# Kernel optimization log

Measured on AMD Instinct MI355X. Metric: run time of the kernel, lower is better.

Reference implementation:

```python
import jax, jax.numpy as jnp
import numpy as np

NUM_SINGERS = 1024
EMB = 63
H = 256
FEAT = 1 + EMB  # 64


def setup_inputs() -> dict:
    key = jax.random.key(0)
    ks = jax.random.split(key, 16)
    B, T = 32, 2048
    s = 0.05
    return {
        "duration_input": jax.random.uniform(ks[0], (B, T), jnp.float32),
        "sid_input": jax.random.randint(ks[1], (B, T), 0, NUM_SINGERS),
        "embed": jax.random.normal(ks[2], (NUM_SINGERS, EMB), jnp.float32) * s,
        "Wi_f": jax.random.normal(ks[3], (FEAT, 3 * H), jnp.float32) * s,
        "Wh_f": jax.random.normal(ks[4], (H, 3 * H), jnp.float32) * s,
        "bi_f": jnp.zeros((3 * H,), jnp.float32),
        "bhn_f": jnp.zeros((H,), jnp.float32),
        "Wi_b": jax.random.normal(ks[5], (FEAT, 3 * H), jnp.float32) * s,
        "Wh_b": jax.random.normal(ks[6], (H, 3 * H), jnp.float32) * s,
        "bi_b": jnp.zeros((3 * H,), jnp.float32),
        "bhn_b": jnp.zeros((H,), jnp.float32),
        "Wd": jax.random.normal(ks[7], (2 * H, 1), jnp.float32) * s,
        "bd": jnp.zeros((1,), jnp.float32),
    }


def _gru(x_tbf, Wi, Wh, bi, bhn):
    # x_tbf: [T, B, F]; flax GRUCell math: r/z recurrent dense without bias,
    # n = tanh(in + r*(Wh_n h + bhn)); h' = (1-z)*n + z*h
    gi = jnp.einsum("tbf,fh->tbh", x_tbf, Wi) + bi  # precompute input gates [T,B,3H]

    def step(h, gi_t):
        gh = h @ Wh  # [B, 3H]
        ir, iz, inn = jnp.split(gi_t, 3, axis=-1)
        hr, hz, hn = jnp.split(gh, 3, axis=-1)
        r = jax.nn.sigmoid(ir + hr)
        z = jax.nn.sigmoid(iz + hz)
        n = jnp.tanh(inn + r * (hn + bhn))
        h_new = (1.0 - z) * n + z * h
        return h_new, h_new

    B = x_tbf.shape[1]
    h0 = jnp.zeros((B, H), x_tbf.dtype)
    _, ys = jax.lax.scan(step, h0, gi)
    return ys  # [T, B, H]


def reference(duration_input, sid_input, embed, Wi_f, Wh_f, bi_f, bhn_f,
              Wi_b, Wh_b, bi_b, bhn_b, Wd, bd):
    sid_emb = embed[sid_input]  # [B, T, EMB]
    feats = jnp.concatenate([duration_input[..., None], sid_emb], axis=-1)  # [B,T,F]
    x = jnp.transpose(feats, (1, 0, 2))  # [T, B, F]
    fwd = _gru(x, Wi_f, Wh_f, bi_f, bhn_f)                 # [T,B,H]
    bwd = _gru(x[::-1], Wi_b, Wh_b, bi_b, bhn_b)[::-1]      # [T,B,H]
    out = jnp.concatenate([fwd, bwd], axis=-1)              # [T,B,2H]
    out = jnp.transpose(out, (1, 0, 2))                     # [B,T,2H]
    return out @ Wd + bd                                    # [B,T,1]
```

## Files before the change

kernel.cpp:

```cpp
#include <hip/hip_runtime.h>
#include <hip/hip_bf16.h>

#define T_LEN 2048
#define BATCH 32
#define HDIM 256
#define H3 768
#define EMBD 63
#define NSING 1024

typedef _Float16 half2_t __attribute__((ext_vector_type(2)));

__device__ __forceinline__ float fdot2u(unsigned int a, unsigned int b, float c) {
  return __builtin_amdgcn_fdot2(__builtin_bit_cast(half2_t, a),
                                __builtin_bit_cast(half2_t, b), c, false);
}

#define DPP_ADD(x, ctrl)                                                      \
  (x) += __builtin_bit_cast(                                                  \
      float, __builtin_amdgcn_update_dpp(                                     \
                 0, __builtin_bit_cast(int, (x)), (ctrl), 0xf, 0xf, true))

__global__ __launch_bounds__(768) void precompute_P(
    const float* __restrict__ embed, const float* __restrict__ Wi,
    const float* __restrict__ bi, _Float16* __restrict__ P2) {
  const int s = blockIdx.x;
  const int jg = threadIdx.x;
  const int g = jg >> 8, jj = jg & 255;
  float acc = bi[jg];
  const float* er = embed + s * EMBD;
#pragma unroll
  for (int e = 0; e < EMBD; e++) acc += er[e] * Wi[(e + 1) * H3 + jg];
  P2[((size_t)g * NSING + s) * HDIM + jj] = (_Float16)acc;
}

__global__ __launch_bounds__(256) void pack_Wh(
    const float* __restrict__ Wh_f, const float* __restrict__ Wh_b,
    unsigned int* __restrict__ Whp) {
  const int bid = blockIdx.x;
  const int j = threadIdx.x;
  const int g = bid % 3;
  const int k2 = (bid / 3) & 63;
  const int half = (bid / 192) & 1;
  const int d = bid / 384;
  const float* Wh = d ? Wh_b : Wh_f;
  const int r0 = half * 128 + 2 * k2;
  half2_t hp;
  hp.x = (_Float16)Wh[r0 * H3 + g * 256 + j];
  hp.y = (_Float16)Wh[(r0 + 1) * H3 + g * 256 + j];
  Whp[(size_t)bid * 256 + j] = __builtin_bit_cast(unsigned int, hp);
}

__global__ __attribute__((amdgpu_flat_work_group_size(512, 512),
                          amdgpu_waves_per_eu(2, 2))) void gru_scan(
    const float* __restrict__ dur, const int* __restrict__ sid,
    const unsigned int* __restrict__ Whp,
    const float* __restrict__ Wi_f, const float* __restrict__ Wi_b,
    const float* __restrict__ bhn_f, const float* __restrict__ bhn_b,
    const float* __restrict__ Wd,
    const _Float16* __restrict__ P2,
    float* __restrict__ pred) {
  const int b = blockIdx.x & 31;
  const int dir = blockIdx.x >> 5;
  const int tid = threadIdx.x;
  const int j = tid & 255;
  const int half = tid >> 8;

  const float* __restrict__ Wi = dir ? Wi_b : Wi_f;
  const float* __restrict__ bhn = dir ? bhn_b : bhn_f;
  const _Float16* __restrict__ Pd = P2 + (size_t)dir * 3 * NSING * HDIM;

  __shared__ __align__(16) unsigned int h2buf[2][128];
  __shared__ float pbuf[3][256];
  
  unsigned int w[192];
  {
    const unsigned int* wp = Whp + ((size_t)(dir * 2 + half)) * 192 * 256 + j;
#pragma unroll
    for (int i = 0; i < 192; i++) w[i] = wp[i * 256];
  }
#pragma unroll
  for (int i = 0; i < 192; i++) asm volatile("" : "+v"(w[i]));

  const float wi0r = Wi[j], wi0z = Wi[HDIM + j], wi0n = Wi[2 * HDIM + j];
  const float wd = Wd[dir * HDIM + j];
  const float bhnj = bhn[j];

  if (tid < 128) h2buf[0][tid] = 0u;
  float h_prev = 0.f;

  const float* durb = dur + b * T_LEN;
  const int* sidb = sid + b * T_LEN;
  float* predb = pred + ((size_t)(dir * BATCH + b)) * T_LEN * 4;

  float p_r = 0.f, p_z = 0.f, p_n = 0.f;
  if (!half) {
    const int s0 = sidb[dir ? (T_LEN - 1) : 0];
    p_r = (float)Pd[(0 * NSING + s0) * HDIM + j];
    p_z = (float)Pd[(1 * NSING + s0) * HDIM + j];
    p_n = (float)Pd[(2 * NSING + s0) * HDIM + j];
  }
  __syncthreads();

#pragma unroll 1
  for (int t = 0; t < T_LEN; t++) {
    const int cur = t & 1;
    const int tt = dir ? (T_LEN - 1 - t) : t;
    const int tn = (t + 1 < T_LEN) ? (t + 1) : (T_LEN - 1);
    float q_r, q_z, q_n;
    if (!half) {
      const int s1 = sidb[dir ? (T_LEN - 1 - tn) : tn];
      q_r = (float)Pd[(0 * NSING + s1) * HDIM + j];
      q_z = (float)Pd[(1 * NSING + s1) * HDIM + j];
      q_n = (float)Pd[(2 * NSING + s1) * HDIM + j];
    }
    const float d_c = durb[tt];

    const uint4* hv4 = (const uint4*)&h2buf[cur][half * 64];
    float ar = 0, az = 0, an = 0, ar2 = 0, az2 = 0, an2 = 0;
#pragma unroll
    for (int kk = 0; kk < 16; kk++) {
      const uint4 hv = hv4[kk];
      const int bi_ = kk * 12;
      ar = fdot2u(hv.x, w[bi_ + 0], ar);
      az = fdot2u(hv.x, w[bi_ + 1], az);
      an = fdot2u(hv.x, w[bi_ + 2], an);
      ar2 = fdot2u(hv.y, w[bi_ + 3], ar2);
      az2 = fdot2u(hv.y, w[bi_ + 4], az2);
      an2 = fdot2u(hv.y, w[bi_ + 5], an2);
      ar = fdot2u(hv.z, w[bi_ + 6], ar);
      az = fdot2u(hv.z, w[bi_ + 7], az);
      an = fdot2u(hv.z, w[bi_ + 8], an);
      ar2 = fdot2u(hv.w, w[bi_ + 9], ar2);
      az2 = fdot2u(hv.w, w[bi_ + 10], az2);
      an2 = fdot2u(hv.w, w[bi_ + 11], an2);
    }
    const float sr = ar + ar2, sz = az + az2, sv = an + an2;

    if (half) {
      pbuf[0][j] = sr;
      pbuf[1][j] = sz;
      pbuf[2][j] = sv;
    }
    __syncthreads();

    if (!half) {
      const float ghr = sr + pbuf[0][j];
      const float ghz = sz + pbuf[1][j];
      const float ghn = sv + pbuf[2][j];
      const float r = 1.f / (1.f + __expf(-(p_r + d_c * wi0r + ghr)));
      const float z = 1.f / (1.f + __expf(-(p_z + d_c * wi0z + ghz)));
      const float nin = p_n + d_c * wi0n + r * (ghn + bhnj);
      const float n = 1.f - 2.f / (1.f + __expf(2.f * nin));
      const float h_new = n + z * (h_prev - n);
      h_prev = h_new;
      ((unsigned short*)&h2buf[cur ^ 1][0])[j] =
          __builtin_bit_cast(unsigned short, (_Float16)h_new);
      float pd = h_new * wd;
      DPP_ADD(pd, 0x111);
      DPP_ADD(pd, 0x112);
      DPP_ADD(pd, 0x114);
      DPP_ADD(pd, 0x118);
      DPP_ADD(pd, 0x142);
      DPP_ADD(pd, 0x143);
      if ((tid & 63) == 63) predb[tt * 4 + (tid >> 6)] = pd;
      p_r = q_r; p_z = q_z; p_n = q_n;
    }
    __syncthreads();
  }
}

__global__ __launch_bounds__(256) void combine(
    const float* __restrict__ pf, const float* __restrict__ pb,
    const float* __restrict__ bd, float* __restrict__ out) {
  const int i = blockIdx.x * 256 + threadIdx.x;
  const float4 a = ((const float4*)pf)[i];
  const float4 c = ((const float4*)pb)[i];
  out[i] = (a.x + a.y + a.z + a.w) + (c.x + c.y + c.z + c.w) + bd[0];
}

extern "C" void kernel_launch(void* const* d_in, const int* in_sizes, int n_in,
                              void* d_out, int out_size, void* d_ws, size_t ws_size,
                              hipStream_t stream) {
  const float* dur = (const float*)d_in[0];
  const int* sid = (const int*)d_in[1];
  const float* embed = (const float*)d_in[2];
  const float* Wi_f = (const float*)d_in[3];
  const float* Wh_f = (const float*)d_in[4];
  const float* bi_f = (const float*)d_in[5];
  const float* bhn_f = (const float*)d_in[6];
  const float* Wi_b = (const float*)d_in[7];
  const float* Wh_b = (const float*)d_in[8];
  const float* bi_b = (const float*)d_in[9];
  const float* bhn_b = (const float*)d_in[10];
  const float* Wd = (const float*)d_in[11];
  const float* bd = (const float*)d_in[12];
  float* out = (float*)d_out;

  float* ws = (float*)d_ws;
  float* pred = ws;
  _Float16* P2 = (_Float16*)(ws + 524288);
  unsigned int* Whp = (unsigned int*)(ws + 524288 + 786432);

  hipLaunchKernelGGL(precompute_P, dim3(NSING), dim3(H3), 0, stream,
                     embed, Wi_f, bi_f, P2);
  hipLaunchKernelGGL(precompute_P, dim3(NSING), dim3(H3), 0, stream,
                     embed, Wi_b, bi_b, P2 + (size_t)3 * NSING * HDIM);
  hipLaunchKernelGGL(pack_Wh, dim3(768), dim3(256), 0, stream, Wh_f, Wh_b, Whp);
  hipLaunchKernelGGL(gru_scan, dim3(64), dim3(512), 0, stream,
                     dur, sid, Whp, Wi_f, Wi_b, bhn_f, bhn_b, Wd, P2, pred);
  hipLaunchKernelGGL(combine, dim3(256), dim3(256), 0, stream,
                     pred, pred + 262144, bd, out);
}
```

Before: 2.537 ms.

## Compute GRU recurrent matvec with MFMA using register- and LDS-resident weight tiles

Replaces the per-thread fdot2 matvec, which used 512 threads split into two K-halves, with 16x16x32 f16 MFMA instructions in a 256-thread block. The recurrent weights are prepacked into MFMA B-fragment layout. 80 tiles per wave stay in VGPRs and the remaining 16 go to LDS. The hidden vector is broadcast as the A operand, so 15 of the 16 rows are wasted work. In exchange the cross-half reduction and the extra threads go away, but register pressure and per-step MFMA latency on the serial path could hurt.

```diff
diff --git a/kernel.cpp b/kernel.cpp
--- a/kernel.cpp
+++ b/kernel.cpp
@@ -8,12 +8,10 @@
 #define EMBD 63
 #define NSING 1024
 
-typedef _Float16 half2_t __attribute__((ext_vector_type(2)));
-
-__device__ __forceinline__ float fdot2u(unsigned int a, unsigned int b, float c) {
-  return __builtin_amdgcn_fdot2(__builtin_bit_cast(half2_t, a),
-                                __builtin_bit_cast(half2_t, b), c, false);
-}
+#define LAYOUT_II 1
+
+typedef _Float16 half8 __attribute__((ext_vector_type(8)));
+typedef float f32x4 __attribute__((ext_vector_type(4)));
 
 #define DPP_ADD(x, ctrl)                                                      \
   (x) += __builtin_bit_cast(                                                  \
@@ -33,27 +31,37 @@
   P2[((size_t)g * NSING + s) * HDIM + jj] = (_Float16)acc;
 }
 
-__global__ __launch_bounds__(256) void pack_Wh(
+__global__ __launch_bounds__(64) void pack_B(
     const float* __restrict__ Wh_f, const float* __restrict__ Wh_b,
-    unsigned int* __restrict__ Whp) {
+    uint4* __restrict__ Bp) {
   const int bid = blockIdx.x;
-  const int j = threadIdx.x;
-  const int g = bid % 3;
-  const int k2 = (bid / 3) & 63;
-  const int half = (bid / 192) & 1;
-  const int d = bid / 384;
-  const float* Wh = d ? Wh_b : Wh_f;
-  const int r0 = half * 128 + 2 * k2;
-  half2_t hp;
-  hp.x = (_Float16)Wh[r0 * H3 + g * 256 + j];
-  hp.y = (_Float16)Wh[(r0 + 1) * H3 + g * 256 + j];
-  Whp[(size_t)bid * 256 + j] = __builtin_bit_cast(unsigned int, hp);
-}
-
-__global__ __attribute__((amdgpu_flat_work_group_size(512, 512),
-                          amdgpu_waves_per_eu(2, 2))) void gru_scan(
+  const int grp = bid / 96, q = bid % 96;
+  const int dir = grp >> 2, w = grp & 3;
+  const int nt = q >> 3, kt = q & 7;
+  const int l = threadIdx.x;
+  const int g = l >> 4;
+  const int j = w * 192 + nt * 16 + (l & 15);
+  const float* Wh = dir ? Wh_b : Wh_f;
+  unsigned int dw[4];
+#pragma unroll
+  for (int r = 0; r < 4; r++) {
+#if LAYOUT_II
+    const int k = kt * 32 + (r >= 2 ? 16 : 0) + g * 4 + (r & 1) * 2;
+#else
+    const int k = kt * 32 + g * 8 + r * 2;
+#endif
+    _Float16 lo = (_Float16)Wh[k * H3 + j];
+    _Float16 hi = (_Float16)Wh[(k + 1) * H3 + j];
+    dw[r] = (unsigned int)__builtin_bit_cast(unsigned short, lo) |
+            ((unsigned int)__builtin_bit_cast(unsigned short, hi) << 16);
+  }
+  Bp[(size_t)bid * 64 + l] = make_uint4(dw[0], dw[1], dw[2], dw[3]);
+}
+
+__global__ __attribute__((amdgpu_flat_work_group_size(256, 256),
+                          amdgpu_waves_per_eu(1, 1))) void gru_scan(
     const float* __restrict__ dur, const int* __restrict__ sid,
-    const unsigned int* __restrict__ Whp,
+    const uint4* __restrict__ Bp,
     const float* __restrict__ Wi_f, const float* __restrict__ Wi_b,
     const float* __restrict__ bhn_f, const float* __restrict__ bhn_b,
     const float* __restrict__ Wd,
@@ -62,109 +70,114 @@
   const int b = blockIdx.x & 31;
   const int dir = blockIdx.x >> 5;
   const int tid = threadIdx.x;
-  const int j = tid & 255;
-  const int half = tid >> 8;
+  const int l = tid & 63;
+  const int w = tid >> 6;
+  const int g = l >> 4;
 
   const float* __restrict__ Wi = dir ? Wi_b : Wi_f;
   const float* __restrict__ bhn = dir ? bhn_b : bhn_f;
   const _Float16* __restrict__ Pd = P2 + (size_t)dir * 3 * NSING * HDIM;
 
-  __shared__ __align__(16) unsigned int h2buf[2][128];
-  __shared__ float pbuf[3][256];
-  
-  unsigned int w[192];
+  __shared__ __align__(16) _Float16 h_lds[HDIM];
+  __shared__ float gh[H3];
+  __shared__ uint4 blds[4][2][8][64];
+
+  uint4 breg[80];
   {
-    const unsigned int* wp = Whp + ((size_t)(dir * 2 + half)) * 192 * 256 + j;
-#pragma unroll
-    for (int i = 0; i < 192; i++) w[i] = wp[i * 256];
-  }
-#pragma unroll
-  for (int i = 0; i < 192; i++) asm volatile("" : "+v"(w[i]));
-
-  const float wi0r = Wi[j], wi0z = Wi[HDIM + j], wi0n = Wi[2 * HDIM + j];
-  const float wd = Wd[dir * HDIM + j];
-  const float bhnj = bhn[j];
-
-  if (tid < 128) h2buf[0][tid] = 0u;
+    const uint4* bp = Bp + ((size_t)(dir * 4 + w) * 96) * 64 + l;
+#pragma unroll
+    for (int q = 0; q < 80; q++) breg[q] = bp[q * 64];
+#pragma unroll
+    for (int q = 80; q < 96; q++)
+      blds[w][(q - 80) >> 3][(q - 80) & 7][l] = bp[q * 64];
+  }
+
+  const float wi0r = Wi[tid], wi0z = Wi[HDIM + tid], wi0n = Wi[2 * HDIM + tid];
+  const float wd = Wd[dir * HDIM + tid];
+  const float bhnj = bhn[tid];
+
+  if (tid < 128) ((unsigned int*)h_lds)[tid] = 0u;
   float h_prev = 0.f;
 
   const float* durb = dur + b * T_LEN;
   const int* sidb = sid + b * T_LEN;
   float* predb = pred + ((size_t)(dir * BATCH + b)) * T_LEN * 4;
 
-  float p_r = 0.f, p_z = 0.f, p_n = 0.f;
-  if (!half) {
+  float p_r, p_z, p_n;
+  {
     const int s0 = sidb[dir ? (T_LEN - 1) : 0];
-    p_r = (float)Pd[(0 * NSING + s0) * HDIM + j];
-    p_z = (float)Pd[(1 * NSING + s0) * HDIM + j];
-    p_n = (float)Pd[(2 * NSING + s0) * HDIM + j];
+    p_r = (float)Pd[(0 * NSING + s0) * HDIM + tid];
+    p_z = (float)Pd[(1 * NSING + s0) * HDIM + tid];
+    p_n = (float)Pd[(2 * NSING + s0) * HDIM + tid];
   }
   __syncthreads();
 
 #pragma unroll 1
   for (int t = 0; t < T_LEN; t++) {
-    const int cur = t & 1;
     const int tt = dir ? (T_LEN - 1 - t) : t;
     const int tn = (t + 1 < T_LEN) ? (t + 1) : (T_LEN - 1);
-    float q_r, q_z, q_n;
-    if (!half) {
-      const int s1 = sidb[dir ? (T_LEN - 1 - tn) : tn];
-      q_r = (float)Pd[(0 * NSING + s1) * HDIM + j];
-      q_z = (float)Pd[(1 * NSING + s1) * HDIM + j];
-      q_n = (float)Pd[(2 * NSING + s1) * HDIM + j];
+    const int s1 = sidb[dir ? (T_LEN - 1 - tn) : tn];
+    const float q_r = (float)Pd[(0 * NSING + s1) * HDIM + tid];
+    const float q_z = (float)Pd[(1 * NSING + s1) * HDIM + tid];
+    const float q_n = (float)Pd[(2 * NSING + s1) * HDIM + tid];
+    const float d_c = durb[tt];
+
+    const char* hb = (const char*)h_lds;
+    half8 a[8];
+#pragma unroll
+    for (int kt = 0; kt < 8; kt++) {
+#if LAYOUT_II
+      const uint2 lo = *(const uint2*)(hb + kt * 64 + g * 8);
+      const uint2 hi = *(const uint2*)(hb + kt * 64 + 32 + g * 8);
+      a[kt] = __builtin_bit_cast(half8, make_uint4(lo.x, lo.y, hi.x, hi.y));
+#else
+      a[kt] = __builtin_bit_cast(half8, *(const uint4*)(hb + kt * 64 + g * 16));
+#endif
     }
-    const float d_c = durb[tt];
-
-    const uint4* hv4 = (const uint4*)&h2buf[cur][half * 64];
-    float ar = 0, az = 0, an = 0, ar2 = 0, az2 = 0, an2 = 0;
-#pragma unroll
-    for (int kk = 0; kk < 16; kk++) {
-      const uint4 hv = hv4[kk];
-      const int bi_ = kk * 12;
-      ar = fdot2u(hv.x, w[bi_ + 0], ar);
-      az = fdot2u(hv.x, w[bi_ + 1], az);
-      an = fdot2u(hv.x, w[bi_ + 2], an);
-      ar2 = fdot2u(hv.y, w[bi_ + 3], ar2);
-      az2 = fdot2u(hv.y, w[bi_ + 4], az2);
-      an2 = fdot2u(hv.y, w[bi_ + 5], an2);
-      ar = fdot2u(hv.z, w[bi_ + 6], ar);
-      az = fdot2u(hv.z, w[bi_ + 7], az);
-      an = fdot2u(hv.z, w[bi_ + 8], an);
-      ar2 = fdot2u(hv.w, w[bi_ + 9], ar2);
-      az2 = fdot2u(hv.w, w[bi_ + 10], az2);
-      an2 = fdot2u(hv.w, w[bi_ + 11], an2);
+
+    f32x4 acc[12];
+#pragma unroll
+    for (int nt = 0; nt < 12; nt++) acc[nt] = (f32x4){0.f, 0.f, 0.f, 0.f};
+#pragma unroll
+    for (int kt = 0; kt < 8; kt++) {
+#pragma unroll
+      for (int nt = 0; nt < 10; nt++)
+        acc[nt] = __builtin_amdgcn_mfma_f32_16x16x32_f16(
+            a[kt], __builtin_bit_cast(half8, breg[nt * 8 + kt]), acc[nt], 0, 0, 0);
+      acc[10] = __builtin_amdgcn_mfma_f32_16x16x32_f16(
+          a[kt], __builtin_bit_cast(half8, blds[w][0][kt][l]), acc[10], 0, 0, 0);
+      acc[11] = __builtin_amdgcn_mfma_f32_16x16x32_f16(
+          a[kt], __builtin_bit_cast(half8, blds[w][1][kt][l]), acc[11], 0, 0, 0);
     }
-    const float sr = ar + ar2, sz = az + az2, sv = an + an2;
-
-    if (half) {
-      pbuf[0][j] = sr;
-      pbuf[1][j] = sz;
-      pbuf[2][j] = sv;
+
+    if (l < 16) {
+#pragma unroll
+      for (int nt = 0; nt < 12; nt++) gh[w * 192 + nt * 16 + l] = acc[nt][0];
     }
     __syncthreads();
 
-    if (!half) {
-      const float ghr = sr + pbuf[0][j];
-      const float ghz = sz + pbuf[1][j];
-      const float ghn = sv + pbuf[2][j];
-      const float r = 1.f / (1.f + __expf(-(p_r + d_c * wi0r + ghr)));
-      const float z = 1.f / (1.f + __expf(-(p_z + d_c * wi0z + ghz)));
-      const float nin = p_n + d_c * wi0n + r * (ghn + bhnj);
-      const float n = 1.f - 2.f / (1.f + __expf(2.f * nin));
-      const float h_new = n + z * (h_prev - n);
-      h_prev = h_new;
-      ((unsigned short*)&h2buf[cur ^ 1][0])[j] =
-          __builtin_bit_cast(unsigned short, (_Float16)h_new);
-      float pd = h_new * wd;
-      DPP_ADD(pd, 0x111);
-      DPP_ADD(pd, 0x112);
-      DPP_ADD(pd, 0x114);
-      DPP_ADD(pd, 0x118);
-      DPP_ADD(pd, 0x142);
-      DPP_ADD(pd, 0x143);
-      if ((tid & 63) == 63) predb[tt * 4 + (tid >> 6)] = pd;
-      p_r = q_r; p_z = q_z; p_n = q_n;
-    }
+    const float ghr = gh[tid];
+    const float ghz = gh[HDIM + tid];
+    const float ghn = gh[2 * HDIM + tid];
+    const float r = 1.f / (1.f + __expf(-(p_r + d_c * wi0r + ghr)));
+    const float z = 1.f / (1.f + __expf(-(p_z + d_c * wi0z + ghz)));
+    const float nin = p_n + d_c * wi0n + r * (ghn + bhnj);
+    const float n = 1.f - 2.f / (1.f + __expf(2.f * nin));
+    const float h_new = n + z * (h_prev - n);
+    h_prev = h_new;
+    ((unsigned short*)h_lds)[tid] =
+        __builtin_bit_cast(unsigned short, (_Float16)h_new);
+
+    float pd = h_new * wd;
+    DPP_ADD(pd, 0x111);
+    DPP_ADD(pd, 0x112);
+    DPP_ADD(pd, 0x114);
+    DPP_ADD(pd, 0x118);
+    DPP_ADD(pd, 0x142);
+    DPP_ADD(pd, 0x143);
+    if (l == 63) predb[tt * 4 + w] = pd;
+
+    p_r = q_r; p_z = q_z; p_n = q_n;
     __syncthreads();
   }
 }
@@ -199,15 +212,15 @@
   float* ws = (float*)d_ws;
   float* pred = ws;
   _Float16* P2 = (_Float16*)(ws + 524288);
-  unsigned int* Whp = (unsigned int*)(ws + 524288 + 786432);
+  uint4* Bp = (uint4*)(ws + 524288 + 786432);
 
   hipLaunchKernelGGL(precompute_P, dim3(NSING), dim3(H3), 0, stream,
                      embed, Wi_f, bi_f, P2);
   hipLaunchKernelGGL(precompute_P, dim3(NSING), dim3(H3), 0, stream,
                      embed, Wi_b, bi_b, P2 + (size_t)3 * NSING * HDIM);
-  hipLaunchKernelGGL(pack_Wh, dim3(768), dim3(256), 0, stream, Wh_f, Wh_b, Whp);
-  hipLaunchKernelGGL(gru_scan, dim3(64), dim3(512), 0, stream,
-                     dur, sid, Whp, Wi_f, Wi_b, bhn_f, bhn_b, Wd, P2, pred);
+  hipLaunchKernelGGL(pack_B, dim3(768), dim3(64), 0, stream, Wh_f, Wh_b, Bp);
+  hipLaunchKernelGGL(gru_scan, dim3(64), dim3(256), 0, stream,
+                     dur, sid, Bp, Wi_f, Wi_b, bhn_f, bhn_b, Wd, P2, pred);
   hipLaunchKernelGGL(combine, dim3(256), dim3(256), 0, stream,
                      pred, pred + 262144, bd, out);
 }
```

New measurement: 3.631 ms. +43.1%, slower.

## Interleave gate projections into half4 table and prefetch next step for all threads

Applied to the files above, without the earlier changes.

The precomputed input-gate table is reorganised so the r, z and n values for a singer/unit sit together as one 8-byte half4 record, letting the scan load them with a single vector load instead of three scattered loads. The next-step sid, duration and gate record are now prefetched by all threads each step. The fdot2 loop is split into blocks separated by sched_barrier, and the asm volatile register pins on the weights are removed. Together these aim to cut per-step gather latency and shape instruction scheduling, at the cost of possible register-allocation changes once the weight pins are gone, and the padding slot adds a little extra traffic.

```diff
diff --git a/kernel.cpp b/kernel.cpp
--- a/kernel.cpp
+++ b/kernel.cpp
@@ -9,6 +9,7 @@
 #define NSING 1024
 
 typedef _Float16 half2_t __attribute__((ext_vector_type(2)));
+typedef _Float16 half4 __attribute__((ext_vector_type(4)));
 
 __device__ __forceinline__ float fdot2u(unsigned int a, unsigned int b, float c) {
   return __builtin_amdgcn_fdot2(__builtin_bit_cast(half2_t, a),
@@ -20,17 +21,22 @@
       float, __builtin_amdgcn_update_dpp(                                     \
                  0, __builtin_bit_cast(int, (x)), (ctrl), 0xf, 0xf, true))
 
-__global__ __launch_bounds__(768) void precompute_P(
+__global__ __launch_bounds__(256) void precompute_P(
     const float* __restrict__ embed, const float* __restrict__ Wi,
-    const float* __restrict__ bi, _Float16* __restrict__ P2) {
+    const float* __restrict__ bi, _Float16* __restrict__ P4) {
   const int s = blockIdx.x;
-  const int jg = threadIdx.x;
-  const int g = jg >> 8, jj = jg & 255;
-  float acc = bi[jg];
+  const int c = threadIdx.x;
+  float ar = bi[c], az = bi[HDIM + c], an = bi[2 * HDIM + c];
   const float* er = embed + s * EMBD;
 #pragma unroll
-  for (int e = 0; e < EMBD; e++) acc += er[e] * Wi[(e + 1) * H3 + jg];
-  P2[((size_t)g * NSING + s) * HDIM + jj] = (_Float16)acc;
+  for (int e = 0; e < EMBD; e++) {
+    const float ev = er[e];
+    ar += ev * Wi[(e + 1) * H3 + c];
+    az += ev * Wi[(e + 1) * H3 + HDIM + c];
+    an += ev * Wi[(e + 1) * H3 + 2 * HDIM + c];
+  }
+  half4 h = {(_Float16)ar, (_Float16)az, (_Float16)an, (_Float16)0.f};
+  *(half4*)(P4 + ((size_t)s * HDIM + c) * 4) = h;
 }
 
 __global__ __launch_bounds__(256) void pack_Wh(
@@ -57,7 +63,7 @@
     const float* __restrict__ Wi_f, const float* __restrict__ Wi_b,
     const float* __restrict__ bhn_f, const float* __restrict__ bhn_b,
     const float* __restrict__ Wd,
-    const _Float16* __restrict__ P2,
+    const _Float16* __restrict__ P4,
     float* __restrict__ pred) {
   const int b = blockIdx.x & 31;
   const int dir = blockIdx.x >> 5;
@@ -66,73 +72,67 @@
   const int half = tid >> 8;
 
   const float* __restrict__ Wi = dir ? Wi_b : Wi_f;
-  const float* __restrict__ bhn = dir ? bhn_b : bhn_f;
-  const _Float16* __restrict__ Pd = P2 + (size_t)dir * 3 * NSING * HDIM;
+  const _Float16* __restrict__ Pdir = P4 + (size_t)dir * NSING * HDIM * 4;
 
   __shared__ __align__(16) unsigned int h2buf[2][128];
   __shared__ float pbuf[3][256];
-  
+
   unsigned int w[192];
   {
     const unsigned int* wp = Whp + ((size_t)(dir * 2 + half)) * 192 * 256 + j;
 #pragma unroll
     for (int i = 0; i < 192; i++) w[i] = wp[i * 256];
   }
-#pragma unroll
-  for (int i = 0; i < 192; i++) asm volatile("" : "+v"(w[i]));
-
-  const float wi0r = Wi[j], wi0z = Wi[HDIM + j], wi0n = Wi[2 * HDIM + j];
+
+  const float wir = Wi[j], wiz = Wi[HDIM + j], win = Wi[2 * HDIM + j];
   const float wd = Wd[dir * HDIM + j];
-  const float bhnj = bhn[j];
+  const float bh = (dir ? bhn_b : bhn_f)[j];
 
   if (tid < 128) h2buf[0][tid] = 0u;
-  float h_prev = 0.f;
+  float hprev = 0.f;
 
   const float* durb = dur + b * T_LEN;
   const int* sidb = sid + b * T_LEN;
   float* predb = pred + ((size_t)(dir * BATCH + b)) * T_LEN * 4;
 
-  float p_r = 0.f, p_z = 0.f, p_n = 0.f;
-  if (!half) {
-    const int s0 = sidb[dir ? (T_LEN - 1) : 0];
-    p_r = (float)Pd[(0 * NSING + s0) * HDIM + j];
-    p_z = (float)Pd[(1 * NSING + s0) * HDIM + j];
-    p_n = (float)Pd[(2 * NSING + s0) * HDIM + j];
-  }
+  const int tt0 = dir ? (T_LEN - 1) : 0;
+  half4 pv = *(const half4*)(Pdir + ((size_t)sidb[tt0] * HDIM + j) * 4);
+  float d_cur = durb[tt0];
   __syncthreads();
 
 #pragma unroll 1
   for (int t = 0; t < T_LEN; t++) {
     const int cur = t & 1;
     const int tt = dir ? (T_LEN - 1 - t) : t;
-    const int tn = (t + 1 < T_LEN) ? (t + 1) : (T_LEN - 1);
-    float q_r, q_z, q_n;
-    if (!half) {
-      const int s1 = sidb[dir ? (T_LEN - 1 - tn) : tn];
-      q_r = (float)Pd[(0 * NSING + s1) * HDIM + j];
-      q_z = (float)Pd[(1 * NSING + s1) * HDIM + j];
-      q_n = (float)Pd[(2 * NSING + s1) * HDIM + j];
-    }
-    const float d_c = durb[tt];
+    const int tn = (t + 1 < T_LEN) ? (t + 1) : t;
+    const int ttn = dir ? (T_LEN - 1 - tn) : tn;
+
+    const int s_nx = sidb[ttn];
+    const float d_nx = durb[ttn];
+    const half4 pv_nx = *(const half4*)(Pdir + ((size_t)s_nx * HDIM + j) * 4);
 
     const uint4* hv4 = (const uint4*)&h2buf[cur][half * 64];
     float ar = 0, az = 0, an = 0, ar2 = 0, az2 = 0, an2 = 0;
 #pragma unroll
-    for (int kk = 0; kk < 16; kk++) {
-      const uint4 hv = hv4[kk];
-      const int bi_ = kk * 12;
-      ar = fdot2u(hv.x, w[bi_ + 0], ar);
-      az = fdot2u(hv.x, w[bi_ + 1], az);
-      an = fdot2u(hv.x, w[bi_ + 2], an);
-      ar2 = fdot2u(hv.y, w[bi_ + 3], ar2);
-      az2 = fdot2u(hv.y, w[bi_ + 4], az2);
-      an2 = fdot2u(hv.y, w[bi_ + 5], an2);
-      ar = fdot2u(hv.z, w[bi_ + 6], ar);
-      az = fdot2u(hv.z, w[bi_ + 7], az);
-      an = fdot2u(hv.z, w[bi_ + 8], an);
-      ar2 = fdot2u(hv.w, w[bi_ + 9], ar2);
-      az2 = fdot2u(hv.w, w[bi_ + 10], az2);
-      an2 = fdot2u(hv.w, w[bi_ + 11], an2);
+    for (int blk = 0; blk < 4; blk++) {
+#pragma unroll
+      for (int kk = blk * 4; kk < blk * 4 + 4; kk++) {
+        const uint4 hv = hv4[kk];
+        const int bi_ = kk * 12;
+        ar = fdot2u(hv.x, w[bi_ + 0], ar);
+        az = fdot2u(hv.x, w[bi_ + 1], az);
+        an = fdot2u(hv.x, w[bi_ + 2], an);
+        ar2 = fdot2u(hv.y, w[bi_ + 3], ar2);
+        az2 = fdot2u(hv.y, w[bi_ + 4], az2);
+        an2 = fdot2u(hv.y, w[bi_ + 5], an2);
+        ar = fdot2u(hv.z, w[bi_ + 6], ar);
+        az = fdot2u(hv.z, w[bi_ + 7], az);
+        an = fdot2u(hv.z, w[bi_ + 8], an);
+        ar2 = fdot2u(hv.w, w[bi_ + 9], ar2);
+        az2 = fdot2u(hv.w, w[bi_ + 10], az2);
+        an2 = fdot2u(hv.w, w[bi_ + 11], an2);
+      }
+      __builtin_amdgcn_sched_barrier(0);
     }
     const float sr = ar + ar2, sz = az + az2, sv = an + an2;
 
@@ -147,12 +147,12 @@
       const float ghr = sr + pbuf[0][j];
       const float ghz = sz + pbuf[1][j];
       const float ghn = sv + pbuf[2][j];
-      const float r = 1.f / (1.f + __expf(-(p_r + d_c * wi0r + ghr)));
-      const float z = 1.f / (1.f + __expf(-(p_z + d_c * wi0z + ghz)));
-      const float nin = p_n + d_c * wi0n + r * (ghn + bhnj);
+      const float r = 1.f / (1.f + __expf(-((float)pv[0] + d_cur * wir + ghr)));
+      const float z = 1.f / (1.f + __expf(-((float)pv[1] + d_cur * wiz + ghz)));
+      const float nin = (float)pv[2] + d_cur * win + r * (ghn + bh);
       const float n = 1.f - 2.f / (1.f + __expf(2.f * nin));
-      const float h_new = n + z * (h_prev - n);
-      h_prev = h_new;
+      const float h_new = n + z * (hprev - n);
+      hprev = h_new;
       ((unsigned short*)&h2buf[cur ^ 1][0])[j] =
           __builtin_bit_cast(unsigned short, (_Float16)h_new);
       float pd = h_new * wd;
@@ -163,9 +163,11 @@
       DPP_ADD(pd, 0x142);
       DPP_ADD(pd, 0x143);
       if ((tid & 63) == 63) predb[tt * 4 + (tid >> 6)] = pd;
-      p_r = q_r; p_z = q_z; p_n = q_n;
     }
     __syncthreads();
+
+    pv = pv_nx;
+    d_cur = d_nx;
   }
 }
 
@@ -197,17 +199,17 @@
   float* out = (float*)d_out;
 
   float* ws = (float*)d_ws;
-  float* pred = ws;
-  _Float16* P2 = (_Float16*)(ws + 524288);
-  unsigned int* Whp = (unsigned int*)(ws + 524288 + 786432);
-
-  hipLaunchKernelGGL(precompute_P, dim3(NSING), dim3(H3), 0, stream,
-                     embed, Wi_f, bi_f, P2);
-  hipLaunchKernelGGL(precompute_P, dim3(NSING), dim3(H3), 0, stream,
-                     embed, Wi_b, bi_b, P2 + (size_t)3 * NSING * HDIM);
+  _Float16* P4 = (_Float16*)ws;
+  unsigned int* Whp = (unsigned int*)(ws + 1048576);
+  float* pred = ws + 1048576 + 196608;
+
+  hipLaunchKernelGGL(precompute_P, dim3(NSING), dim3(256), 0, stream,
+                     embed, Wi_f, bi_f, P4);
+  hipLaunchKernelGGL(precompute_P, dim3(NSING), dim3(256), 0, stream,
+                     embed, Wi_b, bi_b, P4 + (size_t)NSING * HDIM * 4);
   hipLaunchKernelGGL(pack_Wh, dim3(768), dim3(256), 0, stream, Wh_f, Wh_b, Whp);
   hipLaunchKernelGGL(gru_scan, dim3(64), dim3(512), 0, stream,
-                     dur, sid, Whp, Wi_f, Wi_b, bhn_f, bhn_b, Wd, P2, pred);
+                     dur, sid, Whp, Wi_f, Wi_b, bhn_f, bhn_b, Wd, P4, pred);
   hipLaunchKernelGGL(combine, dim3(256), dim3(256), 0, stream,
                      pred, pred + 262144, bd, out);
 }
```

Result: slower. 2.828 ms (+11.5%).
